# Kernel tuning notes

Measured on AMD Instinct MI355X. Metric: run time of the kernel, lower is better.

Reference implementation:

```python
import jax, jax.numpy as jnp
import numpy as np

STRIDES = (8, 16, 32)
REG_MAX = 16
NUM_CLASSES = 80
FMP = ((80, 80), (40, 40), (20, 20))  # 640x640 input / strides


def _anchors(h, w, stride):
    # torch.meshgrid([arange(h), arange(w)]) -> (y, x); stack [x, y]; +0.5; *stride
    ys, xs = jnp.meshgrid(jnp.arange(h, dtype=jnp.float32),
                          jnp.arange(w, dtype=jnp.float32), indexing='ij')
    return (jnp.stack([xs, ys], axis=-1).reshape(-1, 2) + 0.5) * stride  # [H*W, 2]


def _level(cls_feat, reg_feat, cls_w, cls_b, reg_w, reg_b, stride):
    B, _, H, W = cls_feat.shape
    M = H * W
    # 1x1 convs as channel contractions, directly producing NHWC layout
    cls_pred = jnp.einsum('bchw,oc->bhwo', cls_feat, cls_w) + cls_b  # [B,H,W,nc]
    reg_pred = jnp.einsum('bchw,oc->bhwo', reg_feat, reg_w) + reg_b  # [B,H,W,4*reg_max]
    cls_pred = cls_pred.reshape(B, M, NUM_CLASSES)
    reg_pred = reg_pred.reshape(B, M, 4, REG_MAX)
    # DFL: softmax over reg_max bins, project with linspace(0, reg_max, reg_max)
    proj = jnp.linspace(0.0, float(REG_MAX), REG_MAX)
    reg = jnp.einsum('bmfr,r->bmf', jax.nn.softmax(reg_pred, axis=-1), proj)  # [B,M,4]
    anch = _anchors(H, W, stride)  # [M,2], broadcasts over B
    box = jnp.concatenate([anch - reg[..., :2] * stride,
                           anch + reg[..., 2:] * stride], axis=-1)  # [B,M,4]
    return jnp.concatenate([jax.nn.sigmoid(cls_pred), box], axis=-1)  # [B,M,nc+4]


def setup_inputs() -> dict:
    key = jax.random.key(0)
    ks = jax.random.split(key, 18)
    d = {}
    for i, (h, w) in enumerate(FMP):
        d[f'cls_feat{i}'] = jax.random.normal(ks[i], (16, 256, h, w), dtype=jnp.float32)
        d[f'reg_feat{i}'] = jax.random.normal(ks[3 + i], (16, 256, h, w), dtype=jnp.float32)
        d[f'cls_w{i}'] = jax.random.normal(ks[6 + i], (NUM_CLASSES, 256), dtype=jnp.float32) * 0.02
        d[f'cls_b{i}'] = jax.random.normal(ks[9 + i], (NUM_CLASSES,), dtype=jnp.float32) * 0.02
        d[f'reg_w{i}'] = jax.random.normal(ks[12 + i], (4 * REG_MAX, 256), dtype=jnp.float32) * 0.02
        d[f'reg_b{i}'] = jax.random.normal(ks[15 + i], (4 * REG_MAX,), dtype=jnp.float32) * 0.02
    return d


def reference(cls_feat0, cls_feat1, cls_feat2,
              reg_feat0, reg_feat1, reg_feat2,
              cls_w0, cls_w1, cls_w2, cls_b0, cls_b1, cls_b2,
              reg_w0, reg_w1, reg_w2, reg_b0, reg_b1, reg_b2):
    cls_feats = (cls_feat0, cls_feat1, cls_feat2)
    reg_feats = (reg_feat0, reg_feat1, reg_feat2)
    cls_ws = (cls_w0, cls_w1, cls_w2)
    cls_bs = (cls_b0, cls_b1, cls_b2)
    reg_ws = (reg_w0, reg_w1, reg_w2)
    reg_bs = (reg_b0, reg_b1, reg_b2)
    outs = [_level(cls_feats[l], reg_feats[l], cls_ws[l], cls_bs[l],
                   reg_ws[l], reg_bs[l], STRIDES[l]) for l in range(3)]
    return jnp.concatenate(outs, axis=1)  # [B, 8400, nc+4]
```

## Files before the change

### kernel.cpp

```cpp
#include <hip/hip_runtime.h>
#include <hip/hip_bf16.h>
#include <cstdint>

typedef float v4f __attribute__((ext_vector_type(4)));
typedef float v2f __attribute__((ext_vector_type(2)));
typedef short s8v __attribute__((ext_vector_type(8)));
typedef unsigned short u16;

#define WSB_LVL     73728
#define WSB_CLS_SZ  40960
#define BIAS_OFF_B  442368

__device__ __forceinline__ u16 bfbits(float x) {
  return __builtin_bit_cast(u16, __float2bfloat16(x));
}
__device__ __forceinline__ float bff(u16 b) {
  return __builtin_bit_cast(float, ((unsigned int)b) << 16);
}
__device__ __forceinline__ unsigned int packhi(float a, float b) {
  return (unsigned int)bfbits(a) | ((unsigned int)bfbits(b) << 16);
}
__device__ __forceinline__ unsigned int packlo(float a, float b) {
  const float ra = a - bff(bfbits(a));
  const float rb = b - bff(bfbits(b));
  return packhi(ra, rb);
}
__device__ __forceinline__ v4f mfma16(s8v a, s8v b, v4f c) {
  return __builtin_amdgcn_mfma_f32_16x16x32_bf16(a, b, c, 0, 0, 0);
}

__global__ __launch_bounds__(256) void prep_weights(
    const float* __restrict__ cw0, const float* __restrict__ cb0,
    const float* __restrict__ rw0, const float* __restrict__ rb0,
    const float* __restrict__ cw1, const float* __restrict__ cb1,
    const float* __restrict__ rw1, const float* __restrict__ rb1,
    const float* __restrict__ cw2, const float* __restrict__ cb2,
    const float* __restrict__ rw2, const float* __restrict__ rb2,
    void* __restrict__ wsv)
{
  u16* wsB = (u16*)wsv;
  float* biasf = (float*)((char*)wsv + BIAS_OFF_B);
  const int gid = blockIdx.x * 256 + threadIdx.x;
  const float* cws[3] = {cw0, cw1, cw2};
  const float* cbs[3] = {cb0, cb1, cb2};
  const float* rws[3] = {rw0, rw1, rw2};
  const float* rbs[3] = {rb0, rb1, rb2};

  if (gid < 3 * WSB_LVL) {
    const int l = gid / WSB_LVL;
    int r = gid - l * WSB_LVL;
    const bool cls = r < WSB_CLS_SZ;
    if (!cls) r -= WSB_CLS_SZ;
    const int j    = r & 7;
    const int lane = (r >> 3) & 63;
    const int hl   = (r >> 9) & 1;
    int nt, ks;
    if (cls) { const int v = r >> 10; nt = v % 5; ks = v / 5; }
    else     { nt = (r >> 10) & 3; ks = r >> 12; }
    const int o = nt * 16 + (lane & 15);
    const int k = ks * 32 + (lane >> 4) * 8 + j;
    const float* w = cls ? cws[l] : rws[l];
    const float v = w[o * 256 + k];
    u16 bits;
    if (hl == 0) bits = bfbits(v);
    else         bits = bfbits(v - bff(bfbits(v)));
    wsB[gid] = bits;
  } else if (gid < 3 * WSB_LVL + 432) {
    const int i = gid - 3 * WSB_LVL;
    const int l = i / 144;
    const int o = i - l * 144;
    biasf[l * 144 + o] = (o < 80) ? cbs[l][o] : rbs[l][o - 80];
  }
}

template<int NT>
__device__ __forceinline__ void gemm_accum(const float* __restrict__ feat,
                                           const u16* __restrict__ wB,
                                           u16* Abuf, const int t,
                                           const int m0, const int M,
                                           v4f (&acc)[2][NT])
{
  const int kp   = t & 15;
  const int mq0  = t >> 4;
  const int mmA  = min(m0 + mq0 * 4, M - 4);
  const int mmB  = min(m0 + (mq0 + 16) * 4, M - 4);
  const int lane   = t & 63;
  const int lane15 = lane & 15;
  const int kg     = lane >> 4;
  const int mbase  = (t >> 6) * 32;
  unsigned int* AbufW = (unsigned int*)Abuf;
  const int w0 = (mq0 * 4) * 36 + kp;
  const int w1 = ((mq0 + 16) * 4) * 36 + kp;

  v4f r0a = *(const v4f*)(feat + (size_t)(2 * kp) * M + mmA);
  v4f r0b = *(const v4f*)(feat + (size_t)(2 * kp + 1) * M + mmA);
  v4f r1a = *(const v4f*)(feat + (size_t)(2 * kp) * M + mmB);
  v4f r1b = *(const v4f*)(feat + (size_t)(2 * kp + 1) * M + mmB);

#pragma unroll
  for (int ks = 0; ks < 8; ++ks) {
#pragma unroll
    for (int j = 0; j < 4; ++j) {
      AbufW[w0 + j * 36]      = packhi(r0a[j], r0b[j]);
      AbufW[w0 + j * 36 + 16] = packlo(r0a[j], r0b[j]);
      AbufW[w1 + j * 36]      = packhi(r1a[j], r1b[j]);
      AbufW[w1 + j * 36 + 16] = packlo(r1a[j], r1b[j]);
    }
    if (ks < 7) {
      const size_t ko = (size_t)((ks + 1) * 32 + 2 * kp) * M;
      r0a = *(const v4f*)(feat + ko + mmA);
      r0b = *(const v4f*)(feat + ko + M + mmA);
      r1a = *(const v4f*)(feat + ko + mmB);
      r1b = *(const v4f*)(feat + ko + M + mmB);
    }
    __syncthreads();
    const u16* arow0 = Abuf + (mbase + lane15) * 72 + kg * 8;
    const u16* arow1 = Abuf + (mbase + 16 + lane15) * 72 + kg * 8;
    const s8v ahi0 = *(const s8v*)(arow0);
    const s8v alo0 = *(const s8v*)(arow0 + 32);
    const s8v ahi1 = *(const s8v*)(arow1);
    const s8v alo1 = *(const s8v*)(arow1 + 32);
#pragma unroll
    for (int nt = 0; nt < NT; ++nt) {
      const u16* bp = wB + (size_t)((ks * NT + nt) * 2) * 512 + lane * 8;
      const s8v bhi = *(const s8v*)(bp);
      const s8v blo = *(const s8v*)(bp + 512);
      acc[0][nt] = mfma16(ahi0, bhi, acc[0][nt]);
      acc[0][nt] = mfma16(ahi0, blo, acc[0][nt]);
      acc[0][nt] = mfma16(alo0, bhi, acc[0][nt]);
      acc[1][nt] = mfma16(ahi1, bhi, acc[1][nt]);
      acc[1][nt] = mfma16(ahi1, blo, acc[1][nt]);
      acc[1][nt] = mfma16(alo1, bhi, acc[1][nt]);
    }
    __syncthreads();
  }
}

__global__ __launch_bounds__(256, 3) void head_kernel(
    const float* __restrict__ cf0, const float* __restrict__ rf0,
    const float* __restrict__ cf1, const float* __restrict__ rf1,
    const float* __restrict__ cf2, const float* __restrict__ rf2,
    const void* __restrict__ wsv, float* __restrict__ out)
{
  __shared__ __align__(16) char smem[45056];
  u16*  Abuf     = (u16*)smem;
  float* ostage   = (float*)smem;
  float* boxstage = (float*)(smem + 43008);

  const u16*  wsB   = (const u16*)wsv;
  const float* biasf = (const float*)((const char*)wsv + BIAS_OFF_B);

  const int t   = threadIdx.x;
  const int bid = blockIdx.x;

  int l, r;
  if (bid < 800)       { l = 0; r = bid; }
  else if (bid < 1008) { l = 1; r = bid - 800; }
  else                 { l = 2; r = bid - 1008; }

  const int tiles = (l == 0) ? 50 : (l == 1) ? 13 : 4;
  const int M     = (l == 0) ? 6400 : (l == 1) ? 1600 : 400;
  const int W     = (l == 0) ? 80 : (l == 1) ? 40 : 20;
  const int moff  = (l == 0) ? 0 : (l == 1) ? 6400 : 8000;
  const float sv  = (float)(8 << l);

  const int b    = r / tiles;
  const int tile = r - b * tiles;
  const int m0   = tile * 128;

  const float* cfL = (l == 0) ? cf0 : (l == 1) ? cf1 : cf2;
  const float* rfL = (l == 0) ? rf0 : (l == 1) ? rf1 : rf2;
  const float* featR = rfL + (size_t)b * 256 * (size_t)M;
  const float* featC = cfL + (size_t)b * 256 * (size_t)M;
  const u16* wBcls = wsB + l * WSB_LVL;
  const u16* wBreg = wsB + l * WSB_LVL + WSB_CLS_SZ;
  const int loff = l * 144;

  const int lane   = t & 63;
  const int lane15 = lane & 15;
  const int kg     = lane >> 4;
  const int mbase  = (t >> 6) * 32;

  v4f accR[2][4];
#pragma unroll
  for (int mr = 0; mr < 2; ++mr)
#pragma unroll
    for (int nt = 0; nt < 4; ++nt) accR[mr][nt] = (v4f){0.f, 0.f, 0.f, 0.f};
  gemm_accum<4>(featR, wBreg, Abuf, t, m0, M, accR);

  float bR[4];
#pragma unroll
  for (int f = 0; f < 4; ++f) bR[f] = biasf[loff + 80 + f * 16 + lane15];

  float d[2][4][4];
#pragma unroll
  for (int mr = 0; mr < 2; ++mr) {
#pragma unroll
    for (int f = 0; f < 4; ++f) {
#pragma unroll
      for (int rr = 0; rr < 4; ++rr) {
        const float xx = accR[mr][f][rr] + bR[f];
        float mx = xx;
        mx = fmaxf(mx, __shfl_xor(mx, 1));
        mx = fmaxf(mx, __shfl_xor(mx, 2));
        mx = fmaxf(mx, __shfl_xor(mx, 4));
        mx = fmaxf(mx, __shfl_xor(mx, 8));
        const float e = __expf(xx - mx);
        float s = e, wq = e * (float)lane15;
        s += __shfl_xor(s, 1); wq += __shfl_xor(wq, 1);
        s += __shfl_xor(s, 2); wq += __shfl_xor(wq, 2);
        s += __shfl_xor(s, 4); wq += __shfl_xor(wq, 4);
        s += __shfl_xor(s, 8); wq += __shfl_xor(wq, 8);
        d[mr][f][rr] = wq * (16.0f / 15.0f) / s;
      }
    }
  }

#pragma unroll
  for (int mr = 0; mr < 2; ++mr) {
#pragma unroll
    for (int rr = 0; rr < 4; ++rr) {
      if (lane15 == mr * 4 + rr) {
        const int pl = mbase + mr * 16 + kg * 4 + rr;
        const int pg = m0 + pl;
        const int hh = pg / W;
        const int wc = pg - hh * W;
        const float ax = ((float)wc + 0.5f) * sv;
        const float ay = ((float)hh + 0.5f) * sv;
        v4f bb;
        bb[0] = ax - d[mr][0][rr] * sv;
        bb[1] = ay - d[mr][1][rr] * sv;
        bb[2] = ax + d[mr][2][rr] * sv;
        bb[3] = ay + d[mr][3][rr] * sv;
        *(v4f*)&boxstage[pl * 4] = bb;
      }
    }
  }

  v4f accC[2][5];
#pragma unroll
  for (int mr = 0; mr < 2; ++mr)
#pragma unroll
    for (int nt = 0; nt < 5; ++nt) accC[mr][nt] = (v4f){0.f, 0.f, 0.f, 0.f};
  gemm_accum<5>(featC, wBcls, Abuf, t, m0, M, accC);

  float bC[5];
#pragma unroll
  for (int nt = 0; nt < 5; ++nt) bC[nt] = biasf[loff + nt * 16 + lane15];

#pragma unroll
  for (int mr = 0; mr < 2; ++mr)
#pragma unroll
    for (int nt = 0; nt < 5; ++nt)
#pragma unroll
      for (int rr = 0; rr < 4; ++rr) {
        const float z = accC[mr][nt][rr] + bC[nt];
        ostage[(mbase + mr * 16 + kg * 4 + rr) * 84 + nt * 16 + lane15] =
            1.f / (1.f + __expf(-z));
      }
  if (t < 128) {
    const v4f bb = *(const v4f*)&boxstage[t * 4];
    *(v4f*)&ostage[t * 84 + 80] = bb;
  }
  __syncthreads();

  float* const obase = out + ((size_t)b * 8400 + moff + m0) * 84;
#pragma unroll
  for (int i = 0; i < 21; ++i) {
    const int p  = i * 256 + t;
    const int fe = p * 2;
    const int m  = fe / 84;
    if (m0 + m < M) {
      *(v2f*)(obase + fe) = *(const v2f*)&ostage[fe];
    }
  }
}

extern "C" void kernel_launch(void* const* d_in, const int* in_sizes, int n_in,
                              void* d_out, int out_size, void* d_ws, size_t ws_size,
                              hipStream_t stream) {
  const float* cf[3]; const float* rff[3];
  const float* cw[3]; const float* cb[3];
  const float* rw[3]; const float* rb[3];
  for (int i = 0; i < 3; ++i) {
    cf[i]  = (const float*)d_in[i * 6 + 0];
    rff[i] = (const float*)d_in[i * 6 + 1];
    cw[i]  = (const float*)d_in[i * 6 + 2];
    cb[i]  = (const float*)d_in[i * 6 + 3];
    rw[i]  = (const float*)d_in[i * 6 + 4];
    rb[i]  = (const float*)d_in[i * 6 + 5];
  }
  float* o = (float*)d_out;

  prep_weights<<<dim3(866), dim3(256), 0, stream>>>(
      cw[0], cb[0], rw[0], rb[0],
      cw[1], cb[1], rw[1], rb[1],
      cw[2], cb[2], rw[2], rb[2], d_ws);

  head_kernel<<<dim3(1072), dim3(256), 0, stream>>>(
      cf[0], rff[0], cf[1], rff[1], cf[2], rff[2], d_ws, o);
}
```

Baseline: 352.9 us.

## Drop LDS output staging, hoist B-fragment loads, raise occupancy to four blocks

Removes the shared-memory output staging buffer and writes sigmoid scores and box coordinates straight from registers to global memory. This shrinks LDS to the A tile only and allows the launch bound to go from three to four blocks per SM. In the GEMM loop, weight-fragment loads are hoisted ahead of the A-tile packing so they overlap with it. __syncthreads is replaced by an lgkmcnt wait plus a raw barrier, and the MFMA section runs at raised wave priority. The trade-offs are less coalesced direct stores (16 floats per row segment) and higher register pressure from the prefetched fragments under the tighter launch bound.

```diff
diff --git a/kernel.cpp b/kernel.cpp
--- a/kernel.cpp
+++ b/kernel.cpp
@@ -27,6 +27,12 @@
 }
 __device__ __forceinline__ v4f mfma16(s8v a, s8v b, v4f c) {
   return __builtin_amdgcn_mfma_f32_16x16x32_bf16(a, b, c, 0, 0, 0);
+}
+
+__device__ __forceinline__ void block_sync_lgkm() {
+  asm volatile("s_waitcnt lgkmcnt(0)" ::: "memory");
+  __builtin_amdgcn_s_barrier();
+  asm volatile("" ::: "memory");
 }
 
 __global__ __launch_bounds__(256) void prep_weights(
@@ -99,6 +105,13 @@
 
 #pragma unroll
   for (int ks = 0; ks < 8; ++ks) {
+    s8v bh[NT], bl[NT];
+#pragma unroll
+    for (int nt = 0; nt < NT; ++nt) {
+      const u16* bp = wB + (size_t)((ks * NT + nt) * 2) * 512 + lane * 8;
+      bh[nt] = *(const s8v*)(bp);
+      bl[nt] = *(const s8v*)(bp + 512);
+    }
 #pragma unroll
     for (int j = 0; j < 4; ++j) {
       AbufW[w0 + j * 36]      = packhi(r0a[j], r0b[j]);
@@ -113,41 +126,37 @@
       r1a = *(const v4f*)(feat + ko + mmB);
       r1b = *(const v4f*)(feat + ko + M + mmB);
     }
-    __syncthreads();
+    block_sync_lgkm();
     const u16* arow0 = Abuf + (mbase + lane15) * 72 + kg * 8;
     const u16* arow1 = Abuf + (mbase + 16 + lane15) * 72 + kg * 8;
     const s8v ahi0 = *(const s8v*)(arow0);
     const s8v alo0 = *(const s8v*)(arow0 + 32);
     const s8v ahi1 = *(const s8v*)(arow1);
     const s8v alo1 = *(const s8v*)(arow1 + 32);
+    __builtin_amdgcn_s_setprio(1);
 #pragma unroll
     for (int nt = 0; nt < NT; ++nt) {
-      const u16* bp = wB + (size_t)((ks * NT + nt) * 2) * 512 + lane * 8;
-      const s8v bhi = *(const s8v*)(bp);
-      const s8v blo = *(const s8v*)(bp + 512);
-      acc[0][nt] = mfma16(ahi0, bhi, acc[0][nt]);
-      acc[0][nt] = mfma16(ahi0, blo, acc[0][nt]);
-      acc[0][nt] = mfma16(alo0, bhi, acc[0][nt]);
-      acc[1][nt] = mfma16(ahi1, bhi, acc[1][nt]);
-      acc[1][nt] = mfma16(ahi1, blo, acc[1][nt]);
-      acc[1][nt] = mfma16(alo1, bhi, acc[1][nt]);
-    }
-    __syncthreads();
-  }
-}
-
-__global__ __launch_bounds__(256, 3) void head_kernel(
+      acc[0][nt] = mfma16(ahi0, bh[nt], acc[0][nt]);
+      acc[0][nt] = mfma16(ahi0, bl[nt], acc[0][nt]);
+      acc[0][nt] = mfma16(alo0, bh[nt], acc[0][nt]);
+      acc[1][nt] = mfma16(ahi1, bh[nt], acc[1][nt]);
+      acc[1][nt] = mfma16(ahi1, bl[nt], acc[1][nt]);
+      acc[1][nt] = mfma16(alo1, bh[nt], acc[1][nt]);
+    }
+    __builtin_amdgcn_s_setprio(0);
+    block_sync_lgkm();
+  }
+}
+
+__global__ __launch_bounds__(256, 4) void head_kernel(
     const float* __restrict__ cf0, const float* __restrict__ rf0,
     const float* __restrict__ cf1, const float* __restrict__ rf1,
     const float* __restrict__ cf2, const float* __restrict__ rf2,
     const void* __restrict__ wsv, float* __restrict__ out)
 {
-  __shared__ __align__(16) char smem[45056];
-  u16*  Abuf     = (u16*)smem;
-  float* ostage   = (float*)smem;
-  float* boxstage = (float*)(smem + 43008);
-
-  const u16*  wsB   = (const u16*)wsv;
+  __shared__ __align__(16) u16 Abuf[128 * 72];
+
+  const u16*   wsB   = (const u16*)wsv;
   const float* biasf = (const float*)((const char*)wsv + BIAS_OFF_B);
 
   const int t   = threadIdx.x;
@@ -180,6 +189,8 @@
   const int lane15 = lane & 15;
   const int kg     = lane >> 4;
   const int mbase  = (t >> 6) * 32;
+
+  float* const orow0 = out + ((size_t)b * 8400 + moff + m0) * 84;
 
   v4f accR[2][4];
 #pragma unroll
@@ -222,17 +233,19 @@
     for (int rr = 0; rr < 4; ++rr) {
       if (lane15 == mr * 4 + rr) {
         const int pl = mbase + mr * 16 + kg * 4 + rr;
-        const int pg = m0 + pl;
-        const int hh = pg / W;
-        const int wc = pg - hh * W;
-        const float ax = ((float)wc + 0.5f) * sv;
-        const float ay = ((float)hh + 0.5f) * sv;
-        v4f bb;
-        bb[0] = ax - d[mr][0][rr] * sv;
-        bb[1] = ay - d[mr][1][rr] * sv;
-        bb[2] = ax + d[mr][2][rr] * sv;
-        bb[3] = ay + d[mr][3][rr] * sv;
-        *(v4f*)&boxstage[pl * 4] = bb;
+        if (m0 + pl < M) {
+          const int pg = m0 + pl;
+          const int hh = pg / W;
+          const int wc = pg - hh * W;
+          const float ax = ((float)wc + 0.5f) * sv;
+          const float ay = ((float)hh + 0.5f) * sv;
+          v4f bb;
+          bb[0] = ax - d[mr][0][rr] * sv;
+          bb[1] = ay - d[mr][1][rr] * sv;
+          bb[2] = ax + d[mr][2][rr] * sv;
+          bb[3] = ay + d[mr][3][rr] * sv;
+          *(v4f*)(orow0 + (size_t)pl * 84 + 80) = bb;
+        }
       }
     }
   }
@@ -249,29 +262,18 @@
   for (int nt = 0; nt < 5; ++nt) bC[nt] = biasf[loff + nt * 16 + lane15];
 
 #pragma unroll
-  for (int mr = 0; mr < 2; ++mr)
-#pragma unroll
-    for (int nt = 0; nt < 5; ++nt)
-#pragma unroll
-      for (int rr = 0; rr < 4; ++rr) {
-        const float z = accC[mr][nt][rr] + bC[nt];
-        ostage[(mbase + mr * 16 + kg * 4 + rr) * 84 + nt * 16 + lane15] =
-            1.f / (1.f + __expf(-z));
+  for (int mr = 0; mr < 2; ++mr) {
+#pragma unroll
+    for (int rr = 0; rr < 4; ++rr) {
+      const int pl = mbase + mr * 16 + kg * 4 + rr;
+      if (m0 + pl < M) {
+        float* const prow = orow0 + (size_t)pl * 84;
+#pragma unroll
+        for (int nt = 0; nt < 5; ++nt) {
+          const float z = accC[mr][nt][rr] + bC[nt];
+          prow[nt * 16 + lane15] = 1.f / (1.f + __expf(-z));
+        }
       }
-  if (t < 128) {
-    const v4f bb = *(const v4f*)&boxstage[t * 4];
-    *(v4f*)&ostage[t * 84 + 80] = bb;
-  }
-  __syncthreads();
-
-  float* const obase = out + ((size_t)b * 8400 + moff + m0) * 84;
-#pragma unroll
-  for (int i = 0; i < 21; ++i) {
-    const int p  = i * 256 + t;
-    const int fe = p * 2;
-    const int m  = fe / 84;
-    if (m0 + m < M) {
-      *(v2f*)(obase + fe) = *(const v2f*)&ostage[fe];
     }
   }
 }
```

Result: slower. 372.9 us (+5.7%).
